# Kernel optimization log

Measured on AMD Instinct MI355X. Metric: run time of the kernel, lower is better.

Reference implementation:

```python
import jax, jax.numpy as jnp
import numpy as np

D, N_T, N, N_H = 8, 2048, 64, 8
STD_E = 0.02
STD_Q = 0.02


def setup_inputs() -> dict:
    key = jax.random.key(0)
    k1, k2, k3 = jax.random.split(key, 3)
    r_prime = jax.random.normal(k1, (D, N_T, N), dtype=jnp.float32)
    Q = jax.random.normal(k2, (N_H, N, N), dtype=jnp.float32) * STD_Q
    E = jax.random.normal(k3, (N_H, N, N), dtype=jnp.float32) * STD_E
    return {"r_prime": r_prime, "Q": Q, "E": E}


def reference(r_prime, Q, E):
    # r_prime: (b=d, t=n_t, i=n); Q, E: (h, i, j)
    n_t = r_prime.shape[1]
    # Omega[b,h,t,u] = sum_ij r'[b,t,i] Q[h,i,j] r'[b,u,j]
    Qr = jnp.einsum('hij,buj->bhui', Q, r_prime)          # (b, h, u, i)
    Omega = jnp.einsum('bti,bhui->bhtu', r_prime, Qr)     # (b, h, t, u)
    # causal lower-triangular mask (t >= u)
    mask = jnp.tril(jnp.ones((n_t, n_t), dtype=r_prime.dtype))
    Omega = Omega * mask  # broadcast over (b, h)
    # r[b,t,i] = sum_{h,u,j} Omega[b,h,t,u] E[h,i,j] r'[b,u,j]
    Er = jnp.einsum('hij,buj->bhui', E, r_prime)          # (b, h, u, i)
    r = jnp.einsum('bhtu,bhui->bti', Omega, Er)           # (b, t, i)
    return r
```

## Files before the change

### kernel.cpp

```cpp
#include <hip/hip_runtime.h>

#define D_B 8
#define N_T 2048
#define NN  64
#define N_H 8
#define N_C 32

typedef __bf16 bf16;
typedef bf16 bf16x8 __attribute__((ext_vector_type(8)));
typedef bf16 bf16x4 __attribute__((ext_vector_type(4)));
typedef float f32x4 __attribute__((ext_vector_type(4)));

static __device__ __forceinline__ f32x4 mfma16(bf16x8 a, bf16x8 b, f32x4 c) {
    return __builtin_amdgcn_mfma_f32_16x16x32_bf16(a, b, c, 0, 0, 0);
}

__global__ __launch_bounds__(512, 2) void k_pre(
    const float* __restrict__ rp, const float* __restrict__ Qm,
    const float* __restrict__ Em,
    bf16* __restrict__ Qr, bf16* __restrict__ ErT, bf16* __restrict__ Rbf,
    float* __restrict__ dG)
{
    const int c = blockIdx.x, b = blockIdx.y;
    const int tid = threadIdx.x;
    const int w = tid >> 6, l = tid & 63, q = l >> 4, l16 = l & 15;
    const int g = w >> 2, w2 = w & 3;

    __shared__ bf16 Rl[64 * 72];
    __shared__ bf16 Ql[64 * 72];
    __shared__ bf16 El[64 * 72];
    __shared__ bf16 QT[64 * 72];
    __shared__ bf16 ET[64 * 72];

    {
        const int row = tid >> 3, col = (tid & 7) * 8;
        const float* src = rp + ((size_t)(b * N_T) + c * 64 + row) * NN + col;
        bf16x8 v;
#pragma unroll
        for (int k = 0; k < 8; k++) v[k] = (bf16)src[k];
        *(bf16x8*)&Rl[row * 72 + col] = v;
        *(bf16x8*)&Rbf[((size_t)b * N_T + c * 64 + row) * NN + col] = v;
    }

    f32x4 dg0 = {0.f, 0.f, 0.f, 0.f};
    f32x4 dg1 = {0.f, 0.f, 0.f, 0.f};

    for (int h = 0; h < N_H; h++) {
        __syncthreads();
        {
            const int row = tid >> 3, col = (tid & 7) * 8;
            const float* qs = Qm + (size_t)(h * NN + row) * NN + col;
            const float* es = Em + (size_t)(h * NN + row) * NN + col;
            bf16x8 vq, ve;
#pragma unroll
            for (int k = 0; k < 8; k++) { vq[k] = (bf16)qs[k]; ve[k] = (bf16)es[k]; }
            *(bf16x8*)&Ql[row * 72 + col] = vq;
            *(bf16x8*)&El[row * 72 + col] = ve;
        }
        __syncthreads();
        {
            const bf16x8 a0 = *(const bf16x8*)&Rl[(w2 * 16 + l16) * 72 + q * 8];
            const bf16x8 a1 = *(const bf16x8*)&Rl[(w2 * 16 + l16) * 72 + 32 + q * 8];
            const bf16* Bsrc = (g == 0) ? Ql : El;
#pragma unroll
            for (int ns = 0; ns < 4; ns++) {
                const bf16x8 b0 = *(const bf16x8*)&Bsrc[(ns * 16 + l16) * 72 + q * 8];
                const bf16x8 b1 = *(const bf16x8*)&Bsrc[(ns * 16 + l16) * 72 + 32 + q * 8];
                f32x4 z = {0.f, 0.f, 0.f, 0.f};
                f32x4 s = mfma16(a0, b0, z);
                s = mfma16(a1, b1, s);
                bf16x4 p;
#pragma unroll
                for (int r = 0; r < 4; r++) p[r] = (bf16)s[r];
                if (g == 0) {
#pragma unroll
                    for (int r = 0; r < 4; r++) {
                        const int u = c * 64 + w2 * 16 + q * 4 + r;
                        Qr[((size_t)(b * N_H + h) * N_T + u) * NN + ns * 16 + l16] = p[r];
                    }
                    *(bf16x4*)&QT[(ns * 16 + l16) * 72 + w2 * 16 + q * 4] = p;
                } else {
                    *(bf16x4*)&ET[(ns * 16 + l16) * 72 + w2 * 16 + q * 4] = p;
                }
            }
        }
        __syncthreads();
        {
            const bf16x8 a0 = *(const bf16x8*)&QT[(w2 * 16 + l16) * 72 + q * 8];
            const bf16x8 a1 = *(const bf16x8*)&QT[(w2 * 16 + l16) * 72 + 32 + q * 8];
            {
                const int col = g * 32;
                const bf16x8 b0 = *(const bf16x8*)&ET[(col + l16) * 72 + q * 8];
                const bf16x8 b1 = *(const bf16x8*)&ET[(col + l16) * 72 + 32 + q * 8];
                dg0 = mfma16(a0, b0, dg0);
                dg0 = mfma16(a1, b1, dg0);
            }
            {
                const int col = g * 32 + 16;
                const bf16x8 b0 = *(const bf16x8*)&ET[(col + l16) * 72 + q * 8];
                const bf16x8 b1 = *(const bf16x8*)&ET[(col + l16) * 72 + 32 + q * 8];
                dg1 = mfma16(a0, b0, dg1);
                dg1 = mfma16(a1, b1, dg1);
            }
        }
        {
            const int row = tid >> 3, col = (tid & 7) * 8;
            const bf16x8 v = *(const bf16x8*)&ET[row * 72 + col];
            *(bf16x8*)&ErT[((size_t)(b * N_H + h) * NN + row) * N_T + c * 64 + col] = v;
        }
    }
    {
        float* dst = dG + (size_t)(b * N_C + c) * 4096;
#pragma unroll
        for (int r = 0; r < 4; r++) {
            dst[(w2 * 16 + q * 4 + r) * 64 + g * 32 + l16] = dg0[r];
            dst[(w2 * 16 + q * 4 + r) * 64 + g * 32 + 16 + l16] = dg1[r];
        }
    }
}

__global__ __launch_bounds__(256) void k_scan(const float* __restrict__ dG,
                                              bf16* __restrict__ GT)
{
    const int b = blockIdx.x, tid = threadIdx.x;
    __shared__ float T[64 * 65];
    float run[16];
#pragma unroll
    for (int k = 0; k < 16; k++) run[k] = 0.f;
    for (int c = 0; c < N_C; c++) {
        const float* src = dG + (size_t)(b * N_C + c) * 4096;
        float v[16];
#pragma unroll
        for (int k = 0; k < 16; k++) v[k] = src[k * 256 + tid];
#pragma unroll
        for (int k = 0; k < 16; k++) {
            const int idx = k * 256 + tid;
            T[(idx >> 6) * 65 + (idx & 63)] = run[k];
        }
        __syncthreads();
        bf16* dst = GT + (size_t)(b * N_C + c) * 4096;
#pragma unroll
        for (int k = 0; k < 16; k++) {
            const int odx = k * 256 + tid;
            dst[odx] = (bf16)T[(odx & 63) * 65 + (odx >> 6)];
        }
        __syncthreads();
#pragma unroll
        for (int k = 0; k < 16; k++) run[k] += v[k];
    }
}

__global__ __launch_bounds__(512, 2) void k_main(
    const bf16* __restrict__ Qr, const bf16* __restrict__ ErT,
    const bf16* __restrict__ Rbf, const bf16* __restrict__ GT,
    float* __restrict__ out)
{
    const int c = blockIdx.x, b = blockIdx.y;
    const int tid = threadIdx.x;
    const int w = tid >> 6, l = tid & 63, q = l >> 4, l16 = l & 15;
    const int g = w >> 2, s = w & 3;
    const int t0 = c * 64;

    __shared__ bf16 Sl[8 * 16 * 72];
    __shared__ float Ob[4 * 16 * 65];

    bf16* Sw = &Sl[w * 16 * 72];

    const bf16x8 a0 = *(const bf16x8*)&Rbf[((size_t)b * N_T + t0 + s * 16 + l16) * NN + q * 8];
    const bf16x8 a1 = *(const bf16x8*)&Rbf[((size_t)b * N_T + t0 + s * 16 + l16) * NN + 32 + q * 8];

    f32x4 acc[4];
#pragma unroll
    for (int ns = 0; ns < 4; ns++) { f32x4 z = {0.f, 0.f, 0.f, 0.f}; acc[ns] = z; }

    for (int hh = 0; hh < 4; hh++) {
        const int h = g * 4 + hh;
        const bf16* Qrt = Qr + ((size_t)(b * N_H + h) * N_T + t0) * NN;
        const bf16* Ert = ErT + (size_t)(b * N_H + h) * NN * N_T + t0;
#pragma unroll
        for (int ns = 0; ns < 4; ns++) {
            const bf16x8 b0 = *(const bf16x8*)&Qrt[(ns * 16 + l16) * NN + q * 8];
            const bf16x8 b1 = *(const bf16x8*)&Qrt[(ns * 16 + l16) * NN + 32 + q * 8];
            f32x4 z = {0.f, 0.f, 0.f, 0.f};
            f32x4 sv = mfma16(a0, b0, z);
            sv = mfma16(a1, b1, sv);
            const int u_loc = ns * 16 + l16;
#pragma unroll
            for (int r = 0; r < 4; r++) {
                const int t_loc = s * 16 + q * 4 + r;
                const float vv = (u_loc <= t_loc) ? sv[r] : 0.f;
                Sw[(q * 4 + r) * 72 + u_loc] = (bf16)vv;
            }
        }
        const bf16x8 sa0 = *(const bf16x8*)&Sw[l16 * 72 + q * 8];
        const bf16x8 sa1 = *(const bf16x8*)&Sw[l16 * 72 + 32 + q * 8];
#pragma unroll
        for (int ns = 0; ns < 4; ns++) {
            const bf16x8 e0 = *(const bf16x8*)&Ert[(size_t)(ns * 16 + l16) * N_T + q * 8];
            const bf16x8 e1 = *(const bf16x8*)&Ert[(size_t)(ns * 16 + l16) * N_T + 32 + q * 8];
            acc[ns] = mfma16(sa0, e0, acc[ns]);
            acc[ns] = mfma16(sa1, e1, acc[ns]);
        }
    }
    if (g == 1) {
        const bf16* Gt = GT + (size_t)(b * N_C + c) * 4096;
#pragma unroll
        for (int ns = 0; ns < 4; ns++) {
            const bf16x8 g0 = *(const bf16x8*)&Gt[(ns * 16 + l16) * 64 + q * 8];
            const bf16x8 g1 = *(const bf16x8*)&Gt[(ns * 16 + l16) * 64 + 32 + q * 8];
            acc[ns] = mfma16(a0, g0, acc[ns]);
            acc[ns] = mfma16(a1, g1, acc[ns]);
        }
    }
    if (g == 0) {
#pragma unroll
        for (int ns = 0; ns < 4; ns++)
#pragma unroll
            for (int r = 0; r < 4; r++)
                Ob[(s * 16 + q * 4 + r) * 65 + ns * 16 + l16] = acc[ns][r];
    }
    __syncthreads();
    if (g == 1) {
#pragma unroll
        for (int ns = 0; ns < 4; ns++)
#pragma unroll
            for (int r = 0; r < 4; r++) {
                const float sum = acc[ns][r] + Ob[(s * 16 + q * 4 + r) * 65 + ns * 16 + l16];
                out[((size_t)b * N_T + t0 + s * 16 + q * 4 + r) * NN + ns * 16 + l16] = sum;
            }
    }
}

extern "C" void kernel_launch(void* const* d_in, const int* in_sizes, int n_in,
                              void* d_out, int out_size, void* d_ws, size_t ws_size,
                              hipStream_t stream) {
    const float* rp = (const float*)d_in[0];
    const float* Qm = (const float*)d_in[1];
    const float* Em = (const float*)d_in[2];
    float* out = (float*)d_out;

    bf16* Qr = (bf16*)d_ws;
    bf16* ErT = Qr + (size_t)D_B * N_H * N_T * NN;
    bf16* Rbf = ErT + (size_t)D_B * N_H * N_T * NN;
    float* dG = (float*)(Rbf + (size_t)D_B * N_T * NN);
    bf16* GT = (bf16*)(dG + (size_t)D_B * N_C * 4096);

    k_pre<<<dim3(N_C, D_B), 512, 0, stream>>>(rp, Qm, Em, Qr, ErT, Rbf, dG);
    k_scan<<<D_B, 256, 0, stream>>>(dG, GT);
    k_main<<<dim3(N_C, D_B), 512, 0, stream>>>(Qr, ErT, Rbf, GT, out);
}
```

Baseline: 113.2 us.

## Fuse pre, scan and main kernels into one cooperative kernel with grid sync

Merges the three launches into one cooperative kernel that keeps each chunk's Qr tiles in shared memory and uses a grid-wide sync between the chunk-delta phase and the output phase. The serial per-batch scan kernel is replaced by each block summing its predecessor chunk deltas (now stored as bf16) directly. Q/E are read straight from global memory into MFMA operands with vectorized float4 loads instead of being staged through LDS. The aim is to cut launch overhead, the Qr and Rbf round-trips through global memory, and the low-parallelism scan. In exchange it needs about 99 KB of dynamic LDS per block, relies on all 256 blocks being co-resident, does redundant O(c) prefix summation per block, and rounds the deltas to bf16 before summing, which loses some precision.

```diff
diff --git a/kernel.cpp b/kernel.cpp
--- a/kernel.cpp
+++ b/kernel.cpp
@@ -1,4 +1,7 @@
 #include <hip/hip_runtime.h>
+#include <hip/hip_cooperative_groups.h>
+
+namespace cg = cooperative_groups;
 
 #define D_B 8
 #define N_T 2048
@@ -11,96 +14,90 @@
 typedef bf16 bf16x4 __attribute__((ext_vector_type(4)));
 typedef float f32x4 __attribute__((ext_vector_type(4)));
 
+#define SMEM_BYTES 101376
+
 static __device__ __forceinline__ f32x4 mfma16(bf16x8 a, bf16x8 b, f32x4 c) {
     return __builtin_amdgcn_mfma_f32_16x16x32_bf16(a, b, c, 0, 0, 0);
 }
 
-__global__ __launch_bounds__(512, 2) void k_pre(
+static __device__ __forceinline__ bf16x8 ldcvt8(const float* p) {
+    const f32x4 v0 = *(const f32x4*)p;
+    const f32x4 v1 = *(const f32x4*)(p + 4);
+    bf16x8 r;
+#pragma unroll
+    for (int k = 0; k < 4; k++) { r[k] = (bf16)v0[k]; r[4 + k] = (bf16)v1[k]; }
+    return r;
+}
+
+__global__ __launch_bounds__(512, 2) void k_fused(
     const float* __restrict__ rp, const float* __restrict__ Qm,
     const float* __restrict__ Em,
-    bf16* __restrict__ Qr, bf16* __restrict__ ErT, bf16* __restrict__ Rbf,
-    float* __restrict__ dG)
+    bf16* __restrict__ ErT, bf16* __restrict__ dGb, float* __restrict__ out)
 {
+    extern __shared__ char smem[];
+    bf16* Rl  = (bf16*)smem;
+    bf16* Qrl = (bf16*)(smem + 9216);
+    bf16* QT  = (bf16*)(smem + 82944);
+    bf16* ET  = (bf16*)(smem + 92160);
+    bf16* Sl  = (bf16*)(smem + 82944);
+    float* Ob = (float*)(smem + 82944);
+    bf16* Gb  = (bf16*)smem;
+
     const int c = blockIdx.x, b = blockIdx.y;
     const int tid = threadIdx.x;
     const int w = tid >> 6, l = tid & 63, q = l >> 4, l16 = l & 15;
     const int g = w >> 2, w2 = w & 3;
 
-    __shared__ bf16 Rl[64 * 72];
-    __shared__ bf16 Ql[64 * 72];
-    __shared__ bf16 El[64 * 72];
-    __shared__ bf16 QT[64 * 72];
-    __shared__ bf16 ET[64 * 72];
-
     {
         const int row = tid >> 3, col = (tid & 7) * 8;
         const float* src = rp + ((size_t)(b * N_T) + c * 64 + row) * NN + col;
-        bf16x8 v;
-#pragma unroll
-        for (int k = 0; k < 8; k++) v[k] = (bf16)src[k];
-        *(bf16x8*)&Rl[row * 72 + col] = v;
-        *(bf16x8*)&Rbf[((size_t)b * N_T + c * 64 + row) * NN + col] = v;
-    }
+        *(bf16x8*)&Rl[row * 72 + col] = ldcvt8(src);
+    }
+    __syncthreads();
+    const bf16x8 a0 = *(const bf16x8*)&Rl[(w2 * 16 + l16) * 72 + q * 8];
+    const bf16x8 a1 = *(const bf16x8*)&Rl[(w2 * 16 + l16) * 72 + 32 + q * 8];
 
     f32x4 dg0 = {0.f, 0.f, 0.f, 0.f};
     f32x4 dg1 = {0.f, 0.f, 0.f, 0.f};
 
     for (int h = 0; h < N_H; h++) {
+        const float* Bsrc = (g == 0) ? (Qm + (size_t)h * 4096) : (Em + (size_t)h * 4096);
+#pragma unroll
+        for (int ns = 0; ns < 4; ns++) {
+            const bf16x8 b0 = ldcvt8(Bsrc + (ns * 16 + l16) * 64 + q * 8);
+            const bf16x8 b1 = ldcvt8(Bsrc + (ns * 16 + l16) * 64 + 32 + q * 8);
+            f32x4 z = {0.f, 0.f, 0.f, 0.f};
+            f32x4 s = mfma16(a0, b0, z);
+            s = mfma16(a1, b1, s);
+            bf16x4 p;
+#pragma unroll
+            for (int r = 0; r < 4; r++) p[r] = (bf16)s[r];
+            if (g == 0) {
+#pragma unroll
+                for (int r = 0; r < 4; r++)
+                    Qrl[h * 4608 + (w2 * 16 + q * 4 + r) * 72 + ns * 16 + l16] = p[r];
+                *(bf16x4*)&QT[(ns * 16 + l16) * 72 + w2 * 16 + q * 4] = p;
+            } else {
+                *(bf16x4*)&ET[(ns * 16 + l16) * 72 + w2 * 16 + q * 4] = p;
+            }
+        }
         __syncthreads();
         {
-            const int row = tid >> 3, col = (tid & 7) * 8;
-            const float* qs = Qm + (size_t)(h * NN + row) * NN + col;
-            const float* es = Em + (size_t)(h * NN + row) * NN + col;
-            bf16x8 vq, ve;
-#pragma unroll
-            for (int k = 0; k < 8; k++) { vq[k] = (bf16)qs[k]; ve[k] = (bf16)es[k]; }
-            *(bf16x8*)&Ql[row * 72 + col] = vq;
-            *(bf16x8*)&El[row * 72 + col] = ve;
-        }
-        __syncthreads();
-        {
-            const bf16x8 a0 = *(const bf16x8*)&Rl[(w2 * 16 + l16) * 72 + q * 8];
-            const bf16x8 a1 = *(const bf16x8*)&Rl[(w2 * 16 + l16) * 72 + 32 + q * 8];
-            const bf16* Bsrc = (g == 0) ? Ql : El;
-#pragma unroll
-            for (int ns = 0; ns < 4; ns++) {
-                const bf16x8 b0 = *(const bf16x8*)&Bsrc[(ns * 16 + l16) * 72 + q * 8];
-                const bf16x8 b1 = *(const bf16x8*)&Bsrc[(ns * 16 + l16) * 72 + 32 + q * 8];
-                f32x4 z = {0.f, 0.f, 0.f, 0.f};
-                f32x4 s = mfma16(a0, b0, z);
-                s = mfma16(a1, b1, s);
-                bf16x4 p;
-#pragma unroll
-                for (int r = 0; r < 4; r++) p[r] = (bf16)s[r];
-                if (g == 0) {
-#pragma unroll
-                    for (int r = 0; r < 4; r++) {
-                        const int u = c * 64 + w2 * 16 + q * 4 + r;
-                        Qr[((size_t)(b * N_H + h) * N_T + u) * NN + ns * 16 + l16] = p[r];
-                    }
-                    *(bf16x4*)&QT[(ns * 16 + l16) * 72 + w2 * 16 + q * 4] = p;
-                } else {
-                    *(bf16x4*)&ET[(ns * 16 + l16) * 72 + w2 * 16 + q * 4] = p;
-                }
-            }
-        }
-        __syncthreads();
-        {
-            const bf16x8 a0 = *(const bf16x8*)&QT[(w2 * 16 + l16) * 72 + q * 8];
-            const bf16x8 a1 = *(const bf16x8*)&QT[(w2 * 16 + l16) * 72 + 32 + q * 8];
+            const bf16x8 qa0 = *(const bf16x8*)&QT[(w2 * 16 + l16) * 72 + q * 8];
+            const bf16x8 qa1 = *(const bf16x8*)&QT[(w2 * 16 + l16) * 72 + 32 + q * 8];
             {
                 const int col = g * 32;
-                const bf16x8 b0 = *(const bf16x8*)&ET[(col + l16) * 72 + q * 8];
-                const bf16x8 b1 = *(const bf16x8*)&ET[(col + l16) * 72 + 32 + q * 8];
-                dg0 = mfma16(a0, b0, dg0);
-                dg0 = mfma16(a1, b1, dg0);
+                const bf16x8 e0 = *(const bf16x8*)&ET[(col + l16) * 72 + q * 8];
+                const bf16x8 e1 = *(const bf16x8*)&ET[(col + l16) * 72 + 32 + q * 8];
+                dg0 = mfma16(qa0, e0, dg0);
+                dg0 = mfma16(qa1, e1, dg0);
             }
             {
                 const int col = g * 32 + 16;
-                const bf16x8 b0 = *(const bf16x8*)&ET[(col + l16) * 72 + q * 8];
-                const bf16x8 b1 = *(const bf16x8*)&ET[(col + l16) * 72 + 32 + q * 8];
-                dg1 = mfma16(a0, b0, dg1);
-                dg1 = mfma16(a1, b1, dg1);
+                const bf16x8 e0 = *(const bf16x8*)&ET[(col + l16) * 72 + q * 8];
+                const bf16x8 e1 = *(const bf16x8*)&ET[(col + l16) * 72 + 32 + q * 8];
+                dg1 = mfma16(qa0, e0, dg1);
+                dg1 = mfma16(qa1, e1, dg1);
             }
         }
         {
@@ -108,86 +105,55 @@
             const bf16x8 v = *(const bf16x8*)&ET[row * 72 + col];
             *(bf16x8*)&ErT[((size_t)(b * N_H + h) * NN + row) * N_T + c * 64 + col] = v;
         }
+        __syncthreads();
     }
     {
-        float* dst = dG + (size_t)(b * N_C + c) * 4096;
+        bf16* dst = dGb + (size_t)(b * N_C + c) * 4096;
 #pragma unroll
         for (int r = 0; r < 4; r++) {
-            dst[(w2 * 16 + q * 4 + r) * 64 + g * 32 + l16] = dg0[r];
-            dst[(w2 * 16 + q * 4 + r) * 64 + g * 32 + 16 + l16] = dg1[r];
-        }
-    }
-}
-
-__global__ __launch_bounds__(256) void k_scan(const float* __restrict__ dG,
-                                              bf16* __restrict__ GT)
-{
-    const int b = blockIdx.x, tid = threadIdx.x;
-    __shared__ float T[64 * 65];
-    float run[16];
-#pragma unroll
-    for (int k = 0; k < 16; k++) run[k] = 0.f;
-    for (int c = 0; c < N_C; c++) {
-        const float* src = dG + (size_t)(b * N_C + c) * 4096;
-        float v[16];
-#pragma unroll
-        for (int k = 0; k < 16; k++) v[k] = src[k * 256 + tid];
-#pragma unroll
-        for (int k = 0; k < 16; k++) {
-            const int idx = k * 256 + tid;
-            T[(idx >> 6) * 65 + (idx & 63)] = run[k];
-        }
-        __syncthreads();
-        bf16* dst = GT + (size_t)(b * N_C + c) * 4096;
-#pragma unroll
-        for (int k = 0; k < 16; k++) {
-            const int odx = k * 256 + tid;
-            dst[odx] = (bf16)T[(odx & 63) * 65 + (odx >> 6)];
-        }
-        __syncthreads();
-#pragma unroll
-        for (int k = 0; k < 16; k++) run[k] += v[k];
-    }
-}
-
-__global__ __launch_bounds__(512, 2) void k_main(
-    const bf16* __restrict__ Qr, const bf16* __restrict__ ErT,
-    const bf16* __restrict__ Rbf, const bf16* __restrict__ GT,
-    float* __restrict__ out)
-{
-    const int c = blockIdx.x, b = blockIdx.y;
-    const int tid = threadIdx.x;
-    const int w = tid >> 6, l = tid & 63, q = l >> 4, l16 = l & 15;
-    const int g = w >> 2, s = w & 3;
-    const int t0 = c * 64;
-
-    __shared__ bf16 Sl[8 * 16 * 72];
-    __shared__ float Ob[4 * 16 * 65];
-
-    bf16* Sw = &Sl[w * 16 * 72];
-
-    const bf16x8 a0 = *(const bf16x8*)&Rbf[((size_t)b * N_T + t0 + s * 16 + l16) * NN + q * 8];
-    const bf16x8 a1 = *(const bf16x8*)&Rbf[((size_t)b * N_T + t0 + s * 16 + l16) * NN + 32 + q * 8];
-
+            dst[(w2 * 16 + q * 4 + r) * 64 + g * 32 + l16] = (bf16)dg0[r];
+            dst[(w2 * 16 + q * 4 + r) * 64 + g * 32 + 16 + l16] = (bf16)dg1[r];
+        }
+    }
+
+    cg::this_grid().sync();
+
+    {
+        float run[8];
+#pragma unroll
+        for (int k = 0; k < 8; k++) run[k] = 0.f;
+        const bf16* dgbase = dGb + (size_t)b * N_C * 4096 + tid * 8;
+        for (int cp = 0; cp < c; cp++) {
+            const bf16x8 v = *(const bf16x8*)(dgbase + (size_t)cp * 4096);
+#pragma unroll
+            for (int k = 0; k < 8; k++) run[k] += (float)v[k];
+        }
+        const int ip = tid >> 3, ii0 = (tid & 7) * 8;
+#pragma unroll
+        for (int k = 0; k < 8; k++) Gb[(ii0 + k) * 72 + ip] = (bf16)run[k];
+    }
+    __syncthreads();
+
+    bf16* Sw = Sl + w * 1152;
     f32x4 acc[4];
 #pragma unroll
     for (int ns = 0; ns < 4; ns++) { f32x4 z = {0.f, 0.f, 0.f, 0.f}; acc[ns] = z; }
 
     for (int hh = 0; hh < 4; hh++) {
         const int h = g * 4 + hh;
-        const bf16* Qrt = Qr + ((size_t)(b * N_H + h) * N_T + t0) * NN;
-        const bf16* Ert = ErT + (size_t)(b * N_H + h) * NN * N_T + t0;
-#pragma unroll
-        for (int ns = 0; ns < 4; ns++) {
-            const bf16x8 b0 = *(const bf16x8*)&Qrt[(ns * 16 + l16) * NN + q * 8];
-            const bf16x8 b1 = *(const bf16x8*)&Qrt[(ns * 16 + l16) * NN + 32 + q * 8];
+        const bf16* Qh = Qrl + h * 4608;
+        const bf16* Ert = ErT + (size_t)(b * N_H + h) * NN * N_T + c * 64;
+#pragma unroll
+        for (int ns = 0; ns < 4; ns++) {
+            const bf16x8 b0 = *(const bf16x8*)&Qh[(ns * 16 + l16) * 72 + q * 8];
+            const bf16x8 b1 = *(const bf16x8*)&Qh[(ns * 16 + l16) * 72 + 32 + q * 8];
             f32x4 z = {0.f, 0.f, 0.f, 0.f};
             f32x4 sv = mfma16(a0, b0, z);
             sv = mfma16(a1, b1, sv);
             const int u_loc = ns * 16 + l16;
 #pragma unroll
             for (int r = 0; r < 4; r++) {
-                const int t_loc = s * 16 + q * 4 + r;
+                const int t_loc = w2 * 16 + q * 4 + r;
                 const float vv = (u_loc <= t_loc) ? sv[r] : 0.f;
                 Sw[(q * 4 + r) * 72 + u_loc] = (bf16)vv;
             }
@@ -203,30 +169,31 @@
         }
     }
     if (g == 1) {
-        const bf16* Gt = GT + (size_t)(b * N_C + c) * 4096;
-#pragma unroll
-        for (int ns = 0; ns < 4; ns++) {
-            const bf16x8 g0 = *(const bf16x8*)&Gt[(ns * 16 + l16) * 64 + q * 8];
-            const bf16x8 g1 = *(const bf16x8*)&Gt[(ns * 16 + l16) * 64 + 32 + q * 8];
+#pragma unroll
+        for (int ns = 0; ns < 4; ns++) {
+            const bf16x8 g0 = *(const bf16x8*)&Gb[(ns * 16 + l16) * 72 + q * 8];
+            const bf16x8 g1 = *(const bf16x8*)&Gb[(ns * 16 + l16) * 72 + 32 + q * 8];
             acc[ns] = mfma16(a0, g0, acc[ns]);
             acc[ns] = mfma16(a1, g1, acc[ns]);
         }
     }
+    __syncthreads();
     if (g == 0) {
 #pragma unroll
         for (int ns = 0; ns < 4; ns++)
 #pragma unroll
             for (int r = 0; r < 4; r++)
-                Ob[(s * 16 + q * 4 + r) * 65 + ns * 16 + l16] = acc[ns][r];
+                Ob[(w2 * 16 + q * 4 + r) * 65 + ns * 16 + l16] = acc[ns][r];
     }
     __syncthreads();
     if (g == 1) {
+        const int t0 = c * 64;
 #pragma unroll
         for (int ns = 0; ns < 4; ns++)
 #pragma unroll
             for (int r = 0; r < 4; r++) {
-                const float sum = acc[ns][r] + Ob[(s * 16 + q * 4 + r) * 65 + ns * 16 + l16];
-                out[((size_t)b * N_T + t0 + s * 16 + q * 4 + r) * NN + ns * 16 + l16] = sum;
+                const float sum = acc[ns][r] + Ob[(w2 * 16 + q * 4 + r) * 65 + ns * 16 + l16];
+                out[((size_t)b * N_T + t0 + w2 * 16 + q * 4 + r) * NN + ns * 16 + l16] = sum;
             }
     }
 }
@@ -239,13 +206,13 @@
     const float* Em = (const float*)d_in[2];
     float* out = (float*)d_out;
 
-    bf16* Qr = (bf16*)d_ws;
-    bf16* ErT = Qr + (size_t)D_B * N_H * N_T * NN;
-    bf16* Rbf = ErT + (size_t)D_B * N_H * N_T * NN;
-    float* dG = (float*)(Rbf + (size_t)D_B * N_T * NN);
-    bf16* GT = (bf16*)(dG + (size_t)D_B * N_C * 4096);
-
-    k_pre<<<dim3(N_C, D_B), 512, 0, stream>>>(rp, Qm, Em, Qr, ErT, Rbf, dG);
-    k_scan<<<D_B, 256, 0, stream>>>(dG, GT);
-    k_main<<<dim3(N_C, D_B), 512, 0, stream>>>(Qr, ErT, Rbf, GT, out);
-}
+    bf16* ErT = (bf16*)d_ws;
+    bf16* dGb = ErT + (size_t)D_B * N_H * NN * N_T;
+
+    hipFuncSetAttribute((const void*)k_fused,
+                        hipFuncAttributeMaxDynamicSharedMemorySize, SMEM_BYTES);
+    void* args[] = {(void*)&rp, (void*)&Qm, (void*)&Em,
+                    (void*)&ErT, (void*)&dGb, (void*)&out};
+    hipLaunchCooperativeKernel((void*)k_fused, dim3(N_C, D_B), dim3(512),
+                               args, SMEM_BYTES, stream);
+}
```

After: 150.7 us. +33.1%, slower.
